# Performance work log

Hardware: AMD Instinct MI355X
Metric: run time of the kernel (lower is better)

The kernel has to match this reference:

```python
import jax, jax.numpy as jnp
import numpy as np

L, B = 2048, 4096
N_TOPICS = 64
TOP_K = 256


def setup_inputs() -> dict:
    key = jax.random.key(0)
    k1, k2, k3, k4 = jax.random.split(key, 4)
    user_seq = jax.random.normal(k1, (L, B), dtype=jnp.float32)
    target_item = jax.random.normal(k2, (B,), dtype=jnp.float32)
    user_seq_topics = jax.random.randint(k3, (L, B), 0, N_TOPICS, dtype=jnp.int64)
    target_item_topic = jax.random.randint(k4, (B,), 0, N_TOPICS, dtype=jnp.int64)
    return {
        "user_seq": user_seq,
        "target_item": target_item,
        "user_seq_topics": user_seq_topics,
        "target_item_topic": target_item_topic,
        "top_k": TOP_K,
    }


def reference(user_seq, target_item, user_seq_topics, target_item_topic, top_k):
    # Vectorized stream compaction per column (batch element).
    Lseq = user_seq.shape[0]
    mask = user_seq_topics == target_item_topic[None, :]  # (L, B)
    # Matched positions keep their original index; unmatched pushed to the end.
    pos = jnp.arange(Lseq, dtype=jnp.int32)[:, None]       # (L, 1)
    sort_key = jnp.where(mask, pos, Lseq)                   # (L, B)
    order = jnp.argsort(sort_key, axis=0)[:top_k]           # (top_k, B) stable-in-order
    gathered = jnp.take_along_axis(user_seq, order, axis=0)  # (top_k, B)
    valid = jnp.take_along_axis(mask, order, axis=0)         # (top_k, B)
    shrunk_user_seq = jnp.where(valid, gathered, jnp.zeros((), user_seq.dtype))
    return shrunk_user_seq
```

## Files before the change

kernel.cpp:

```cpp
#include <hip/hip_runtime.h>


#define NCH 64
#define CPB 16

__global__ __launch_bounds__(1024) void simhs_kernel(
    const float* __restrict__ user_seq,
    const int*   __restrict__ topics,
    const int*   __restrict__ tgt_topic,
    float*       __restrict__ out,
    int L, int B, int K, int chunkRows)
{
    __shared__ int s_cnt[NCH][CPB];

    const int t   = threadIdx.x;
    const int ci  = t & (CPB - 1);
    const int ch  = t >> 4;
    const int col = blockIdx.x * CPB + ci;
    const bool colOK = (col < B);

    if (colOK) {
        for (int k = ch; k < K; k += NCH)
            out[(size_t)k * B + col] = 0.0f;
    }

    const int tt = colOK ? tgt_topic[col] : -1;

    const int r0 = ch * chunkRows;
    const int r1 = (r0 + chunkRows < L) ? (r0 + chunkRows) : L;

    unsigned long long m0 = 0ull;
    if (colOK) {
        const int* tp = topics + col;
        #pragma unroll 16
        for (int r = r0; r < r1; ++r) {
            int v = tp[(size_t)r * B];
            unsigned long long bit = (v == tt) ? 1ull : 0ull;
            m0 |= bit << (r - r0);
        }
    }
    int cnt = __popcll(m0);
    s_cnt[ch][ci] = cnt;
    __syncthreads();

    #pragma unroll
    for (int d = 1; d < NCH; d <<= 1) {
        int v   = s_cnt[ch][ci];
        int add = (ch >= d) ? s_cnt[ch - d][ci] : 0;
        __syncthreads();
        s_cnt[ch][ci] = v + add;
        __syncthreads();
    }

    if (colOK) {
        int base = s_cnt[ch][ci] - cnt;
        const float* us = user_seq + col;
        unsigned long long m = m0;
        while (m) {
            if (base >= K) break;
            int lr = __ffsll(m) - 1;
            m &= m - 1;
            int r = r0 + lr;
            out[(size_t)base * B + col] = us[(size_t)r * B];
            ++base;
        }
    }
}

extern "C" void kernel_launch(void* const* d_in, const int* in_sizes, int n_in,
                              void* d_out, int out_size, void* d_ws, size_t ws_size,
                              hipStream_t stream) {
    const float* user_seq = (const float*)d_in[0];
    const int* topics = (const int*)d_in[2];
    const int* tgt    = (const int*)d_in[3];

    const int B = in_sizes[1];
    const int L = in_sizes[0] / B;
    const int K = out_size / B;
    const int chunkRows = (L + NCH - 1) / NCH;

    const int grid = (B + CPB - 1) / CPB;

    simhs_kernel<<<grid, 1024, 0, stream>>>(
        user_seq, topics, tgt, (float*)d_out, L, B, K, chunkRows);
}
```

Measured before the change: 103.7 us.

## Replace shared-memory barrier scan with wavefront shuffle scan and finer row chunks

Result: slower. 114.9 us (+10.8%).

```diff
diff --git a/kernel.cpp b/kernel.cpp
--- a/kernel.cpp
+++ b/kernel.cpp
@@ -1,22 +1,26 @@
 #include <hip/hip_runtime.h>
 
 
-#define NCH 64
-#define CPB 16
+#define NCH 128
+#define CPB 8
+#define BLOCK (NCH * CPB)
 
-__global__ __launch_bounds__(1024) void simhs_kernel(
+template <int CHUNK>
+__global__ __launch_bounds__(BLOCK) void simhs_kernel(
     const float* __restrict__ user_seq,
     const int*   __restrict__ topics,
     const int*   __restrict__ tgt_topic,
     float*       __restrict__ out,
-    int L, int B, int K, int chunkRows)
+    int L, int B, int K)
 {
-    __shared__ int s_cnt[NCH][CPB];
+    __shared__ int s_tot[BLOCK / 64][CPB];
 
-    const int t   = threadIdx.x;
-    const int ci  = t & (CPB - 1);
-    const int ch  = t >> 4;
-    const int col = blockIdx.x * CPB + ci;
+    const int t    = threadIdx.x;
+    const int ci   = t & (CPB - 1);
+    const int ch   = t >> 3;
+    const int w    = t >> 6;
+    const int lane = t & 63;
+    const int col  = blockIdx.x * CPB + ci;
     const bool colOK = (col < B);
 
     if (colOK) {
@@ -25,43 +29,40 @@
     }
 
     const int tt = colOK ? tgt_topic[col] : -1;
+    const int r0 = ch * CHUNK;
 
-    const int r0 = ch * chunkRows;
-    const int r1 = (r0 + chunkRows < L) ? (r0 + chunkRows) : L;
-
-    unsigned long long m0 = 0ull;
+    unsigned int m = 0u;
     if (colOK) {
-        const int* tp = topics + col;
-        #pragma unroll 16
-        for (int r = r0; r < r1; ++r) {
-            int v = tp[(size_t)r * B];
-            unsigned long long bit = (v == tt) ? 1ull : 0ull;
-            m0 |= bit << (r - r0);
+        const int* tp = topics + (size_t)r0 * B + col;
+        #pragma unroll
+        for (int i = 0; i < CHUNK; ++i) {
+            if (r0 + i < L) {
+                int v = tp[(size_t)i * B];
+                m |= (v == tt ? 1u : 0u) << i;
+            }
         }
     }
-    int cnt = __popcll(m0);
-    s_cnt[ch][ci] = cnt;
+    const int cnt = __popc(m);
+
+    int incl = cnt;
+    #pragma unroll
+    for (int d = 8; d < 64; d <<= 1) {
+        int tmp = __shfl(incl, lane - d, 64);
+        if (lane >= d) incl += tmp;
+    }
+    if (lane >= 56) s_tot[w][lane & (CPB - 1)] = incl;
     __syncthreads();
 
-    #pragma unroll
-    for (int d = 1; d < NCH; d <<= 1) {
-        int v   = s_cnt[ch][ci];
-        int add = (ch >= d) ? s_cnt[ch - d][ci] : 0;
-        __syncthreads();
-        s_cnt[ch][ci] = v + add;
-        __syncthreads();
-    }
+    int base = incl - cnt;
+    for (int w2 = 0; w2 < w; ++w2) base += s_tot[w2][ci];
 
     if (colOK) {
-        int base = s_cnt[ch][ci] - cnt;
         const float* us = user_seq + col;
-        unsigned long long m = m0;
         while (m) {
             if (base >= K) break;
-            int lr = __ffsll(m) - 1;
+            int lr = __ffs(m) - 1;
             m &= m - 1;
-            int r = r0 + lr;
-            out[(size_t)base * B + col] = us[(size_t)r * B];
+            out[(size_t)base * B + col] = us[(size_t)(r0 + lr) * B];
             ++base;
         }
     }
@@ -81,6 +82,10 @@
 
     const int grid = (B + CPB - 1) / CPB;
 
-    simhs_kernel<<<grid, 1024, 0, stream>>>(
-        user_seq, topics, tgt, (float*)d_out, L, B, K, chunkRows);
+    if (chunkRows <= 16)
+        simhs_kernel<16><<<grid, BLOCK, 0, stream>>>(
+            user_seq, topics, tgt, (float*)d_out, L, B, K);
+    else
+        simhs_kernel<32><<<grid, BLOCK, 0, stream>>>(
+            user_seq, topics, tgt, (float*)d_out, L, B, K);
 }
```

## Split into mask-build and gather kernels with 32-row bitmask words

Applied to the files above, without the earlier changes.

Result: no change. 103.0 us (-0.6%).

```diff
diff --git a/kernel.cpp b/kernel.cpp
--- a/kernel.cpp
+++ b/kernel.cpp
@@ -1,69 +1,74 @@
 #include <hip/hip_runtime.h>
 
 
-#define NCH 64
-#define CPB 16
+#define WORD_ROWS 32
 
-__global__ __launch_bounds__(1024) void simhs_kernel(
+__global__ __launch_bounds__(256) void simhs_mask_kernel(
+    const int* __restrict__ topics,
+    const int* __restrict__ tgt_topic,
+    unsigned int* __restrict__ mask,
+    int L, int B, int W)
+{
+    const int tid = blockIdx.x * blockDim.x + threadIdx.x;
+    if (tid >= W * B) return;
+    const int c = tid % B;
+    const int w = tid / B;
+    const int tt = tgt_topic[c];
+    const int r0 = w * WORD_ROWS;
+    const int* tp = topics + (size_t)r0 * B + c;
+
+    unsigned int m = 0u;
+    if (r0 + WORD_ROWS <= L) {
+        int v[WORD_ROWS];
+        #pragma unroll
+        for (int i = 0; i < WORD_ROWS; ++i)
+            v[i] = tp[(size_t)i * B];
+        #pragma unroll
+        for (int i = 0; i < WORD_ROWS; ++i)
+            m |= (v[i] == tt ? 1u : 0u) << i;
+    } else {
+        for (int i = 0; r0 + i < L; ++i)
+            m |= (tp[(size_t)i * B] == tt ? 1u : 0u) << i;
+    }
+    mask[tid] = m;
+}
+
+__global__ __launch_bounds__(256) void simhs_gather_kernel(
     const float* __restrict__ user_seq,
-    const int*   __restrict__ topics,
-    const int*   __restrict__ tgt_topic,
-    float*       __restrict__ out,
-    int L, int B, int K, int chunkRows)
+    const unsigned int* __restrict__ mask,
+    float* __restrict__ out,
+    int B, int K, int W, int KPT)
 {
-    __shared__ int s_cnt[NCH][CPB];
+    const int tid = blockIdx.x * blockDim.x + threadIdx.x;
+    if (tid >= W * B) return;
+    const int c = tid % B;
+    const int w = tid / B;
 
-    const int t   = threadIdx.x;
-    const int ci  = t & (CPB - 1);
-    const int ch  = t >> 4;
-    const int col = blockIdx.x * CPB + ci;
-    const bool colOK = (col < B);
-
-    if (colOK) {
-        for (int k = ch; k < K; k += NCH)
-            out[(size_t)k * B + col] = 0.0f;
+    unsigned int mym = 0u;
+    int base = 0, total = 0;
+    #pragma unroll 8
+    for (int w2 = 0; w2 < W; ++w2) {
+        unsigned int mm = mask[(size_t)w2 * B + c];
+        if (w2 == w) { mym = mm; base = total; }
+        total += __popc(mm);
     }
 
-    const int tt = colOK ? tgt_topic[col] : -1;
-
-    const int r0 = ch * chunkRows;
-    const int r1 = (r0 + chunkRows < L) ? (r0 + chunkRows) : L;
-
-    unsigned long long m0 = 0ull;
-    if (colOK) {
-        const int* tp = topics + col;
-        #pragma unroll 16
-        for (int r = r0; r < r1; ++r) {
-            int v = tp[(size_t)r * B];
-            unsigned long long bit = (v == tt) ? 1ull : 0ull;
-            m0 |= bit << (r - r0);
-        }
-    }
-    int cnt = __popcll(m0);
-    s_cnt[ch][ci] = cnt;
-    __syncthreads();
-
+    const int k0 = w * KPT;
     #pragma unroll
-    for (int d = 1; d < NCH; d <<= 1) {
-        int v   = s_cnt[ch][ci];
-        int add = (ch >= d) ? s_cnt[ch - d][ci] : 0;
-        __syncthreads();
-        s_cnt[ch][ci] = v + add;
-        __syncthreads();
+    for (int j = 0; j < 4; ++j) {
+        int k = k0 + j;
+        if (j < KPT && k < K && k >= total)
+            out[(size_t)k * B + c] = 0.0f;
     }
 
-    if (colOK) {
-        int base = s_cnt[ch][ci] - cnt;
-        const float* us = user_seq + col;
-        unsigned long long m = m0;
-        while (m) {
-            if (base >= K) break;
-            int lr = __ffsll(m) - 1;
-            m &= m - 1;
-            int r = r0 + lr;
-            out[(size_t)base * B + col] = us[(size_t)r * B];
-            ++base;
-        }
+    const float* us = user_seq + c;
+    const int r0 = w * WORD_ROWS;
+    while (mym) {
+        if (base >= K) break;
+        int lr = __ffs(mym) - 1;
+        mym &= mym - 1;
+        out[(size_t)base * B + c] = us[(size_t)(r0 + lr) * B];
+        ++base;
     }
 }
 
@@ -77,10 +82,15 @@
     const int B = in_sizes[1];
     const int L = in_sizes[0] / B;
     const int K = out_size / B;
-    const int chunkRows = (L + NCH - 1) / NCH;
+    const int W = (L + WORD_ROWS - 1) / WORD_ROWS;
+    const int KPT = (K + W - 1) / W;
 
-    const int grid = (B + CPB - 1) / CPB;
+    unsigned int* mask = (unsigned int*)d_ws;
 
-    simhs_kernel<<<grid, 1024, 0, stream>>>(
-        user_seq, topics, tgt, (float*)d_out, L, B, K, chunkRows);
+    const int total_threads = W * B;
+    const int grid = (total_threads + 255) / 256;
+
+    simhs_mask_kernel<<<grid, 256, 0, stream>>>(topics, tgt, mask, L, B, W);
+    simhs_gather_kernel<<<grid, 256, 0, stream>>>(user_seq, mask, (float*)d_out,
+                                                  B, K, W, KPT);
 }
```
